# Kernel optimization log

Measured on AMD Instinct MI355X. Metric: run time of the kernel, lower is better.

## Reference

```python
import jax, jax.numpy as jnp
import numpy as np

RESO = 64            # plane_resolution
PADDING = 0.1
HID = 128            # hidden_dim
CDIM = 128           # c_dim
NBLOCKS = 5
PLANES = ((0, 2), (0, 1), (1, 2))  # xz, xy, yz column picks


def _plane_index(p, cols):
    # normalize_coordinate + coordinate2index (2d)
    xy = p[..., list(cols)] / (1.0 + PADDING + 1e-3) + 0.5
    xy = jnp.clip(xy, 0.0, 1.0 - 1e-3)
    ij = (xy * RESO).astype(jnp.int32)
    return ij[..., 0] + RESO * ij[..., 1]  # [B, T]


def _flat_idx(idx, S):
    B = idx.shape[0]
    return (idx + jnp.arange(B, dtype=idx.dtype)[:, None] * S).reshape(-1)


def _scatter_max(src, idx, S):
    # src [B,T,F], idx [B,T] -> [B,S,F]; empty bins -> 0 (torch_scatter convention)
    B, T, F = src.shape
    m = jax.ops.segment_max(src.reshape(B * T, F), _flat_idx(idx, S), num_segments=B * S)
    m = jnp.where(jnp.isfinite(m), m, jnp.zeros((), src.dtype))
    return m.reshape(B, S, F)


def _scatter_mean(src, idx, S):
    B, T, F = src.shape
    flat = _flat_idx(idx, S)
    s = jax.ops.segment_sum(src.reshape(B * T, F), flat, num_segments=B * S)
    cnt = jax.ops.segment_sum(jnp.ones((B * T,), src.dtype), flat, num_segments=B * S)
    return (s / jnp.maximum(cnt, 1.0)[:, None]).reshape(B, S, F)


def _resblock(x, w0, b0, w1, b1, ws):
    # ONet ResnetBlockFC: fc_1(relu(fc_0(relu(x)))) + shortcut(x)
    net = jax.nn.relu(x) @ w0 + b0
    dx = jax.nn.relu(net) @ w1 + b1
    return x @ ws + dx


def setup_inputs() -> dict:
    key = jax.random.key(0)
    ks = jax.random.split(key, 10)
    sc = 0.05
    return {
        "p": jax.random.normal(ks[0], (8, 20000, 3), dtype=jnp.float32),
        "fc_pos_w": jax.random.normal(ks[1], (3, 2 * HID), dtype=jnp.float32) * sc,
        "fc_pos_b": jnp.zeros((2 * HID,), jnp.float32),
        "blk0_w": jax.random.normal(ks[2], (NBLOCKS, 2 * HID, HID), dtype=jnp.float32) * sc,
        "blk0_b": jnp.zeros((NBLOCKS, HID), jnp.float32),
        "blk1_w": jax.random.normal(ks[3], (NBLOCKS, HID, HID), dtype=jnp.float32) * sc,
        "blk1_b": jnp.zeros((NBLOCKS, HID), jnp.float32),
        "blk_sc_w": jax.random.normal(ks[4], (NBLOCKS, 2 * HID, HID), dtype=jnp.float32) * sc,
        "fc_c_w": jax.random.normal(ks[5], (HID, CDIM), dtype=jnp.float32) * sc,
        "fc_c_b": jnp.zeros((CDIM,), jnp.float32),
    }


def reference(p, fc_pos_w, fc_pos_b, blk0_w, blk0_b, blk1_w, blk1_b, blk_sc_w, fc_c_w, fc_c_b):
    S = RESO * RESO
    B = p.shape[0]
    idxs = [_plane_index(p, cols) for cols in PLANES]

    net = p @ fc_pos_w + fc_pos_b                         # [B,T,2H]
    net = _resblock(net, blk0_w[0], blk0_b[0], blk1_w[0], blk1_b[0], blk_sc_w[0])
    for i in range(1, NBLOCKS):
        pooled = jnp.zeros_like(net[..., :HID])
        for idx in idxs:
            fea = _scatter_max(net, idx, S)               # [B,S,H]
            pooled = pooled + jnp.take_along_axis(fea, idx[:, :, None], axis=1)
        net = jnp.concatenate([net, pooled], axis=-1)     # [B,T,2H]
        net = _resblock(net, blk0_w[i], blk0_b[i], blk1_w[i], blk1_b[i], blk_sc_w[i])

    c = net @ fc_c_w + fc_c_b                             # [B,T,C]
    feas = []
    for idx in idxs:
        fp = _scatter_mean(c, idx, S)                     # [B,S,C]
        feas.append(fp.transpose(0, 2, 1).reshape(B, CDIM, RESO, RESO))
    return jnp.stack(feas)                                # [3,B,C,R,R] (xz, xy, yz)
```

## Files before the change

### kernel.cpp

```cpp
#include <hip/hip_runtime.h>
#include <cstdint>
#include <cstddef>

#define NP     160000
#define NB     8
#define TPB    20000
#define H      128
#define SS     4096
#define NCHUNK 625
#define NBLK   10
#define PPB    2000

typedef _Float16 half8  __attribute__((ext_vector_type(8)));
typedef _Float16 half4v __attribute__((ext_vector_type(4)));
typedef float    f32x16 __attribute__((ext_vector_type(16)));

__device__ __forceinline__ half8 reluh8(half8 x) {
  half8 z = (half8)(_Float16)0;
  return __builtin_elementwise_max(x, z);
}

__global__ __launch_bounds__(256) void k_hist(const float* __restrict__ p,
                                              int* __restrict__ idx,
                                              unsigned* __restrict__ hist) {
  __shared__ unsigned lh[SS];
  const int tid = threadIdx.x;
  const int plb = blockIdx.x % 24;
  const int blk = blockIdx.x / 24;
  const int pl = plb >> 3, b = plb & 7;
  for (int j = tid; j < SS; j += 256) lh[j] = 0;
  __syncthreads();
  const float DEN = (float)(1.0 + 0.1 + 1e-3);
  const float HI  = (float)(1.0 - 1e-3);
  const int nbase = b*TPB + blk*PPB;
  for (int j = tid; j < PPB; j += 256) {
    const int n = nbase + j;
    const float px = p[3*n], py = p[3*n+1], pz = p[3*n+2];
    float ca, cb;
    if (pl == 0)      { ca = px; cb = pz; }
    else if (pl == 1) { ca = px; cb = py; }
    else              { ca = py; cb = pz; }
    const float na = fminf(fmaxf(ca / DEN + 0.5f, 0.0f), HI);
    const float nb = fminf(fmaxf(cb / DEN + 0.5f, 0.0f), HI);
    const int bin = (int)(na * 64.0f) + 64 * (int)(nb * 64.0f);
    idx[pl*NP + n] = bin;
    atomicAdd(&lh[bin], 1u);
  }
  __syncthreads();
  unsigned* dst = hist + ((size_t)plb*NBLK + blk)*SS;
  for (int j = tid; j < SS; j += 256) dst[j] = lh[j];
}

__global__ __launch_bounds__(256) void k_scan2(unsigned* __restrict__ hist,
                                               unsigned* __restrict__ cnt,
                                               int* __restrict__ cursor) {
  __shared__ unsigned stot[SS];
  __shared__ unsigned ssum[256];
  __shared__ unsigned sbase[256];
  const int plb = blockIdx.x;
  const int tid = threadIdx.x;
  unsigned* hp = hist + (size_t)plb*NBLK*SS;
  for (int j = tid; j < SS; j += 256) {
    unsigned t = 0;
    #pragma unroll
    for (int blk = 0; blk < NBLK; ++blk) t += hp[blk*SS + j];
    stot[j] = t;
  }
  __syncthreads();
  unsigned local = 0;
  #pragma unroll
  for (int i = 0; i < 16; ++i) local += stot[tid*16 + i];
  ssum[tid] = local;
  __syncthreads();
  if (tid == 0) {
    unsigned run = 0;
    for (int i = 0; i < 256; ++i) { sbase[i] = run; run += ssum[i]; }
  }
  __syncthreads();
  unsigned run = sbase[tid];
  for (int i = 0; i < 16; ++i) {
    const int bin = tid*16 + i;
    const unsigned tot = stot[bin];
    cnt[plb*SS + bin] = tot;
    cursor[plb*SS + bin] = (int)(run + tot);
    unsigned acc = run;
    #pragma unroll
    for (int blk = 0; blk < NBLK; ++blk) {
      const unsigned c = hp[blk*SS + bin];
      hp[blk*SS + bin] = acc;
      acc += c;
    }
    run += tot;
  }
}

__global__ __launch_bounds__(256) void k_reorder2(const int* __restrict__ idx,
                                                  const unsigned* __restrict__ hist,
                                                  int* __restrict__ order) {
  __shared__ unsigned lrank[SS];
  const int tid = threadIdx.x;
  const int plb = blockIdx.x % 24;
  const int blk = blockIdx.x / 24;
  const int pl = plb >> 3, b = plb & 7;
  for (int j = tid; j < SS; j += 256) lrank[j] = 0;
  __syncthreads();
  const unsigned* bp = hist + ((size_t)plb*NBLK + blk)*SS;
  int* op = order + pl*NP + b*TPB;
  const int nbase = b*TPB + blk*PPB;
  for (int j = tid; j < PPB; j += 256) {
    const int n = nbase + j;
    const int bin = idx[pl*NP + n];
    const unsigned r = atomicAdd(&lrank[bin], 1u);
    op[bp[bin] + r] = (bin << 18) | n;
  }
}

__global__ __launch_bounds__(256) void k_wconv(const float* __restrict__ w0,
                                               const float* __restrict__ w1,
                                               const float* __restrict__ wsc,
                                               _Float16* __restrict__ wb) {
  int t = blockIdx.x*256 + threadIdx.x;
  if (t >= 51200) return;
  int L = t / 10240, r = t % 10240;
  const float* src; _Float16* dst; int q;
  if (r < 4096)      { q = r;        src = w0  + L*32768; dst = wb + L*81920;         }
  else if (r < 8192) { q = r - 4096; src = wsc + L*32768; dst = wb + L*81920 + 32768; }
  else               { q = r - 8192; src = w1  + L*16384; dst = wb + L*81920 + 65536; }
  int kt = q >> 8, nt = (q >> 6) & 3, l = q & 63;
  int k0 = kt*16 + ((l >> 5) << 3);
  int n  = nt*32 + (l & 31);
  union { _Float16 h[8]; uint4 u; } o;
  #pragma unroll
  for (int j = 0; j < 8; ++j) o.h[j] = (_Float16)src[(size_t)(k0 + j)*H + n];
  *(uint4*)(dst + (size_t)q*8) = o.u;
}

template<int OP>
__global__ __launch_bounds__(256) void k_poolA(const _Float16* __restrict__ net,
                                               const int* __restrict__ order,
                                               _Float16* __restrict__ fea,
                                               float* __restrict__ sums,
                                               float* __restrict__ pbufF,
                                               float* __restrict__ pbufL) {
  const int tid   = threadIdx.x;
  const int plb   = blockIdx.x % 24;
  const int chunk = (blockIdx.x / 24) * 8 + (tid >> 5);
  if (chunk >= NCHUNK) return;
  const int gi = tid & 31, f4 = gi << 2;
  const int pl = plb >> 3, b = plb & 7;
  const int base = pl*NP + b*TPB + chunk*32;
  const int pkv = order[base + gi];
  const int prevbin = (chunk > 0)          ? (order[base - 1] >> 18) : -1;
  const int nextbin = (chunk < NCHUNK - 1) ? (order[base + 32] >> 18) : -1;

  uint2 v[32];
  #pragma unroll
  for (int i = 0; i < 32; ++i) {
    const int pk = __shfl(pkv, i, 32);
    v[i] = *(const uint2*)&net[(size_t)(pk & 0x3FFFF)*H + f4];
  }
  __builtin_amdgcn_sched_barrier(0);

  const size_t pslot = ((size_t)plb*NCHUNK + chunk)*H + f4;
  int cur = __shfl(pkv, 0, 32) >> 18;
  int segstart = 0;
  float a0, a1, a2, a3;
  if (OP == 0) { a0 = a1 = a2 = a3 = -3.0e38f; } else { a0 = a1 = a2 = a3 = 0.f; }

  #pragma unroll
  for (int i = 0; i < 32; ++i) {
    const int bin = __shfl(pkv, i, 32) >> 18;
    if (bin != cur) {
      const bool contin = (segstart == 0) && (prevbin == cur);
      if (!contin) {
        if (OP == 0) {
          union { _Float16 h[4]; uint2 u; } o;
          o.h[0]=(_Float16)a0; o.h[1]=(_Float16)a1; o.h[2]=(_Float16)a2; o.h[3]=(_Float16)a3;
          *(uint2*)&fea[((size_t)plb*SS + cur)*H + f4] = o.u;
        } else {
          *(float4*)&sums[((size_t)plb*SS + cur)*H + f4] = make_float4(a0,a1,a2,a3);
        }
      } else {
        *(float4*)&pbufF[pslot] = make_float4(a0,a1,a2,a3);
      }
      cur = bin; segstart = i;
      if (OP == 0) { a0 = a1 = a2 = a3 = -3.0e38f; } else { a0 = a1 = a2 = a3 = 0.f; }
    }
    union { uint2 u; _Float16 h[4]; } w;
    w.u = v[i];
    if (OP == 0) {
      a0 = fmaxf(a0, (float)w.h[0]); a1 = fmaxf(a1, (float)w.h[1]);
      a2 = fmaxf(a2, (float)w.h[2]); a3 = fmaxf(a3, (float)w.h[3]);
    } else {
      a0 += (float)w.h[0]; a1 += (float)w.h[1];
      a2 += (float)w.h[2]; a3 += (float)w.h[3];
    }
  }
  const bool contin = (segstart == 0) && (prevbin == cur);
  const bool extend = (nextbin == cur);
  if (!contin && !extend) {
    if (OP == 0) {
      union { _Float16 h[4]; uint2 u; } o;
      o.h[0]=(_Float16)a0; o.h[1]=(_Float16)a1; o.h[2]=(_Float16)a2; o.h[3]=(_Float16)a3;
      *(uint2*)&fea[((size_t)plb*SS + cur)*H + f4] = o.u;
    } else {
      *(float4*)&sums[((size_t)plb*SS + cur)*H + f4] = make_float4(a0,a1,a2,a3);
    }
  } else if (contin) {
    *(float4*)&pbufF[pslot] = make_float4(a0,a1,a2,a3);
  } else {
    *(float4*)&pbufL[pslot] = make_float4(a0,a1,a2,a3);
  }
}

template<int OP>
__global__ __launch_bounds__(256) void k_poolB(const int* __restrict__ order,
                                               const int* __restrict__ cursor,
                                               _Float16* __restrict__ fea,
                                               float* __restrict__ sums,
                                               const float* __restrict__ pbufF,
                                               const float* __restrict__ pbufL) {
  const int tid = threadIdx.x;
  const int plb = blockIdx.x % 24;
  const int bnd = (blockIdx.x / 24) * 8 + (tid >> 5);
  if (bnd >= NCHUNK - 1) return;
  const int gi = tid & 31, f4 = gi << 2;
  const int pl = plb >> 3, b = plb & 7;
  const int base = pl*NP + b*TPB;
  const int pos  = (bnd + 1) * 32;
  const int binR = order[base + pos] >> 18;
  const int binL = order[base + pos - 1] >> 18;
  if (binL != binR) return;
  const int beta = binR;
  const int e = cursor[plb*SS + beta];
  const int s = (beta > 0) ? cursor[plb*SS + beta - 1] : 0;
  const int cs = s >> 5, ce = (e - 1) >> 5;
  if (cs != bnd) return;
  float4 acc = *(const float4*)&pbufL[((size_t)plb*NCHUNK + cs)*H + f4];
  #pragma unroll 4
  for (int c = cs + 1; c <= ce; ++c) {
    const float4 q = *(const float4*)&pbufF[((size_t)plb*NCHUNK + c)*H + f4];
    if (OP == 0) {
      acc.x = fmaxf(acc.x, q.x); acc.y = fmaxf(acc.y, q.y);
      acc.z = fmaxf(acc.z, q.z); acc.w = fmaxf(acc.w, q.w);
    } else {
      acc.x += q.x; acc.y += q.y; acc.z += q.z; acc.w += q.w;
    }
  }
  if (OP == 0) {
    union { _Float16 h[4]; uint2 u; } o;
    o.h[0]=(_Float16)acc.x; o.h[1]=(_Float16)acc.y;
    o.h[2]=(_Float16)acc.z; o.h[3]=(_Float16)acc.w;
    *(uint2*)&fea[((size_t)plb*SS + beta)*H + f4] = o.u;
  } else {
    *(float4*)&sums[((size_t)plb*SS + beta)*H + f4] = acc;
  }
}

template<int MODE>
__global__ __launch_bounds__(512, 6) void k_block(
    const float* __restrict__ p,
    const float* __restrict__ wpos, const float* __restrict__ bpos,
    _Float16* __restrict__ net,
    const _Float16* __restrict__ fea, const int* __restrict__ idx,
    const _Float16* __restrict__ wb,
    const float* __restrict__ b0, const float* __restrict__ b1)
{
  __shared__ char smem[49152];
  char* Xs = smem;
  char* Hs = smem + 32768;
  const int tid = threadIdx.x;
  const int n0  = blockIdx.x * 64;

  if (MODE == 0) {
    for (int j = tid; j < 64*64; j += 512) {
      int pt = j >> 6, k4 = (j & 63) << 2;
      int n = n0 + pt;
      float px = p[3*n], py = p[3*n+1], pz = p[3*n+2];
      float4 a  = *(const float4*)&bpos[k4];
      float4 wx = *(const float4*)&wpos[k4];
      float4 wy = *(const float4*)&wpos[256 + k4];
      float4 wz = *(const float4*)&wpos[512 + k4];
      a.x += px*wx.x + py*wy.x + pz*wz.x;
      a.y += px*wx.y + py*wy.y + pz*wz.y;
      a.z += px*wx.z + py*wy.z + pz*wz.z;
      a.w += px*wx.w + py*wy.w + pz*wz.w;
      union { _Float16 h[4]; uint2 u; } o;
      o.h[0] = (_Float16)a.x; o.h[1] = (_Float16)a.y;
      o.h[2] = (_Float16)a.z; o.h[3] = (_Float16)a.w;
      *(uint2*)(Xs + ((pt*512 + k4*2) ^ ((pt & 31) << 4))) = o.u;
    }
  } else {
    for (int j = tid; j < 64*32; j += 512) {
      int pt = j >> 5, k4 = (j & 31) << 2;
      int n = n0 + pt;
      int b = n / TPB;
      uint2 vleft = *(const uint2*)&net[(size_t)n*H + k4];
      union { uint2 u; half4v h; } w0g, w1g, w2g, o;
      w0g.u = *(const uint2*)&fea[(((size_t)(0*NB + b))*SS + idx[0*NP + n])*H + k4];
      w1g.u = *(const uint2*)&fea[(((size_t)(1*NB + b))*SS + idx[1*NP + n])*H + k4];
      w2g.u = *(const uint2*)&fea[(((size_t)(2*NB + b))*SS + idx[2*NP + n])*H + k4];
      o.h = (w0g.h + w1g.h) + w2g.h;
      const int sw = (pt & 31) << 4;
      *(uint2*)(Xs + ((pt*512 + k4*2) ^ sw)) = vleft;
      *(uint2*)(Xs + ((pt*512 + 256 + k4*2) ^ sw)) = o.u;
    }
  }
  __syncthreads();

  const int w  = tid >> 6;
  const int c  = w & 3;
  const int r  = w >> 2;
  const int ln = tid & 63;
  const int l5 = ln >> 5;
  const int lr = ln & 31;
  const int swx   = lr << 4;
  const int xbase = lr*512 + l5*16 + r*16384;
  const int col   = c*32 + lr;
  const _Float16* wb0 = wb;
  const _Float16* wbs = wb + 32768;
  const _Float16* wb1 = wb + 65536;

  f32x16 aR = {};
  #pragma unroll 4
  for (int kt = 0; kt < 16; ++kt) {
    half8 x  = *(const half8*)(Xs + ((xbase + kt*32) ^ swx));
    half8 rx = reluh8(x);
    half8 bw = *(const half8*)(wb0 + ((kt*4 + c)*64 + ln)*8);
    aR = __builtin_amdgcn_mfma_f32_32x32x16_f16(rx, bw, aR, 0, 0, 0);
  }
  const float bb0 = b0[col];
  #pragma unroll
  for (int reg = 0; reg < 16; ++reg) {
    const int ro  = (reg & 3) + 8*(reg >> 2) + 4*l5;
    const int row = r*32 + ro;
    const float v = fmaxf(aR[reg] + bb0, 0.f);
    *(_Float16*)(Hs + ((row*256 + col*2) ^ ((row & 15) << 4))) = (_Float16)v;
  }

  f32x16 aS = {};
  #pragma unroll 4
  for (int kt = 0; kt < 16; ++kt) {
    half8 x  = *(const half8*)(Xs + ((xbase + kt*32) ^ swx));
    half8 bs = *(const half8*)(wbs + ((kt*4 + c)*64 + ln)*8);
    aS = __builtin_amdgcn_mfma_f32_32x32x16_f16(x, bs, aS, 0, 0, 0);
  }
  __syncthreads();

  const int hbase = (r*32 + lr)*256 + l5*16;
  const int swh   = (lr & 15) << 4;
  #pragma unroll 2
  for (int kt = 0; kt < 8; ++kt) {
    half8 h  = *(const half8*)(Hs + ((hbase + kt*32) ^ swh));
    half8 bf = *(const half8*)(wb1 + ((kt*4 + c)*64 + ln)*8);
    aS = __builtin_amdgcn_mfma_f32_32x32x16_f16(h, bf, aS, 0, 0, 0);
  }

  const float bb1 = b1[col];
  #pragma unroll
  for (int reg = 0; reg < 16; ++reg) {
    const int ro = (reg & 3) + 8*(reg >> 2) + 4*l5;
    net[(size_t)(n0 + r*32 + ro)*H + col] = (_Float16)(aS[reg] + bb1);
  }
}

__global__ __launch_bounds__(256) void k_out2(const float* __restrict__ sums,
                                              const unsigned* __restrict__ cnt,
                                              const float* __restrict__ wc,
                                              const float* __restrict__ bc,
                                              float* __restrict__ out) {
  __shared__ float xa[64][132];
  const int plb = blockIdx.y;
  const int s0  = blockIdx.x << 6;
  const int tid = threadIdx.x;

  for (int j = tid; j < 64*32; j += 256) {
    int si = j >> 5, k4 = (j & 31) << 2;
    int s = s0 + si;
    float4 v = *(const float4*)&sums[((size_t)plb*SS + s)*H + k4];
    unsigned c = cnt[(size_t)plb*SS + s];
    float m = (c > 0u) ? (1.0f / (float)c) : 0.0f;
    xa[si][k4+0] = v.x*m; xa[si][k4+1] = v.y*m;
    xa[si][k4+2] = v.z*m; xa[si][k4+3] = v.w*m;
  }
  __syncthreads();

  const int fg = tid & 31;
  const int pg = tid >> 5;
  const int f4c = fg << 2;
  const int prow = pg << 3;
  float ac[8][4];
  #pragma unroll
  for (int i = 0; i < 8; ++i) { ac[i][0]=ac[i][1]=ac[i][2]=ac[i][3]=0.f; }
  #pragma unroll 4
  for (int k = 0; k < H; ++k) {
    const float4 wv = *(const float4*)&wc[(size_t)k*H + f4c];
    #pragma unroll
    for (int i = 0; i < 8; ++i) {
      const float xv = xa[prow + i][k];
      ac[i][0] += xv*wv.x; ac[i][1] += xv*wv.y; ac[i][2] += xv*wv.z; ac[i][3] += xv*wv.w;
    }
  }
  __syncthreads();
  const float4 bv = *(const float4*)&bc[f4c];
  #pragma unroll
  for (int i = 0; i < 8; ++i) {
    float4 o;
    o.x = ac[i][0] + bv.x;
    o.y = ac[i][1] + bv.y;
    o.z = ac[i][2] + bv.z;
    o.w = ac[i][3] + bv.w;
    *(float4*)&xa[prow + i][f4c] = o;
  }
  __syncthreads();

  for (int j = tid; j < H * 16; j += 256) {
    const int ch = j >> 4;
    const int s4 = (j & 15) << 2;
    float4 o;
    o.x = xa[s4 + 0][ch];
    o.y = xa[s4 + 1][ch];
    o.z = xa[s4 + 2][ch];
    o.w = xa[s4 + 3][ch];
    *(float4*)&out[((size_t)plb*H + ch)*SS + s0 + s4] = o;
  }
}

extern "C" void kernel_launch(void* const* d_in, const int* in_sizes, int n_in,
                              void* d_out, int out_size, void* d_ws, size_t ws_size,
                              hipStream_t stream) {
  (void)in_sizes; (void)n_in; (void)out_size; (void)ws_size;
  const float* p      = (const float*)d_in[0];
  const float* wpos   = (const float*)d_in[1];
  const float* bpos   = (const float*)d_in[2];
  const float* blk0w  = (const float*)d_in[3];
  const float* blk0b  = (const float*)d_in[4];
  const float* blk1w  = (const float*)d_in[5];
  const float* blk1b  = (const float*)d_in[6];
  const float* blkscw = (const float*)d_in[7];
  const float* wc     = (const float*)d_in[8];
  const float* bc     = (const float*)d_in[9];
  float* out = (float*)d_out;

  char* ws = (char*)d_ws;
  _Float16* net  = (_Float16*)ws;
  int* idx       = (int*)(ws + 40960000);
  int* order     = (int*)(ws + 42880000);
  int* cursor    = (int*)(ws + 44800000);
  unsigned* cnt  = (unsigned*)(ws + 45193216);
  _Float16* wb   = (_Float16*)(ws + 45586432);
  float* sums    = (float*)(ws + 46405632);
  float* pbufF   = (float*)(ws + 96737280);
  float* pbufL   = (float*)(ws + 104417280);
  unsigned* hist = (unsigned*)(ws + 112097280);
  _Float16* fea  = (_Float16*)d_out;

  k_hist<<<24*NBLK, 256, 0, stream>>>(p, idx, hist);
  k_scan2<<<24, 256, 0, stream>>>(hist, cnt, cursor);
  k_reorder2<<<24*NBLK, 256, 0, stream>>>(idx, hist, order);
  k_wconv<<<200, 256, 0, stream>>>(blk0w, blk1w, blkscw, wb);

  k_block<0><<<2500, 512, 0, stream>>>(p, wpos, bpos, net, nullptr, idx,
                                       wb, blk0b, blk1b);

  for (int i = 1; i < 5; ++i) {
    k_poolA<0><<<79*24, 256, 0, stream>>>(net, order, fea, nullptr, pbufF, pbufL);
    k_poolB<0><<<78*24, 256, 0, stream>>>(order, cursor, fea, nullptr, pbufF, pbufL);
    k_block<1><<<2500, 512, 0, stream>>>(nullptr, nullptr, nullptr, net, fea, idx,
                                         wb + (size_t)i*81920,
                                         blk0b + (size_t)i*H,
                                         blk1b + (size_t)i*H);
  }

  k_poolA<1><<<79*24, 256, 0, stream>>>(net, order, nullptr, sums, pbufF, pbufL);
  k_poolB<1><<<78*24, 256, 0, stream>>>(order, cursor, nullptr, sums, pbufF, pbufL);
  k_out2<<<dim3(64, 24), 256, 0, stream>>>(sums, cnt, wc, bc, out);
}
```

Measured before the change: 470.7 us.

## Make pooled resblock kernel persistent with register prefetch of next tile's gathers

The MODE 1 resblock kernel becomes a persistent kernel launched with 512 blocks that loop over the 2500 point tiles. While the MFMA work for the current tile runs, each thread loads the next tile's net rows and the three gathered plane features into registers. This is meant to hide the latency of those random gathers behind compute. Per-thread constants are hoisted out of the loop and the launch-bounds occupancy hint drops from 6 to 4, which raises register pressure and can leave tiles unevenly spread across blocks.

```diff
diff --git a/kernel.cpp b/kernel.cpp
--- a/kernel.cpp
+++ b/kernel.cpp
@@ -10,6 +10,8 @@
 #define NCHUNK 625
 #define NBLK   10
 #define PPB    2000
+#define NTILE  2500
+#define GRID1  512
 
 typedef _Float16 half8  __attribute__((ext_vector_type(8)));
 typedef _Float16 half4v __attribute__((ext_vector_type(4)));
@@ -258,7 +260,7 @@
 }
 
 template<int MODE>
-__global__ __launch_bounds__(512, 6) void k_block(
+__global__ __launch_bounds__(512, 4) void k_block(
     const float* __restrict__ p,
     const float* __restrict__ wpos, const float* __restrict__ bpos,
     _Float16* __restrict__ net,
@@ -270,9 +272,63 @@
   char* Xs = smem;
   char* Hs = smem + 32768;
   const int tid = threadIdx.x;
-  const int n0  = blockIdx.x * 64;
+
+  const int w  = tid >> 6;
+  const int c  = w & 3;
+  const int r  = w >> 2;
+  const int ln = tid & 63;
+  const int l5 = ln >> 5;
+  const int lr = ln & 31;
+  const int swx   = lr << 4;
+  const int xbase = lr*512 + l5*16 + r*16384;
+  const int col   = c*32 + lr;
+  const int hbase = (r*32 + lr)*256 + l5*16;
+  const int swh   = (lr & 15) << 4;
+  const float bb0 = b0[col];
+  const float bb1 = b1[col];
+  const _Float16* wb0 = wb;
+  const _Float16* wbs = wb + 32768;
+  const _Float16* wb1 = wb + 65536;
+
+  auto COMPUTE = [&](int n0) {
+    f32x16 aR = {};
+    #pragma unroll 4
+    for (int kt = 0; kt < 16; ++kt) {
+      half8 x  = *(const half8*)(Xs + ((xbase + kt*32) ^ swx));
+      half8 rx = reluh8(x);
+      half8 bw = *(const half8*)(wb0 + ((kt*4 + c)*64 + ln)*8);
+      aR = __builtin_amdgcn_mfma_f32_32x32x16_f16(rx, bw, aR, 0, 0, 0);
+    }
+    #pragma unroll
+    for (int reg = 0; reg < 16; ++reg) {
+      const int ro  = (reg & 3) + 8*(reg >> 2) + 4*l5;
+      const int row = r*32 + ro;
+      const float v = fmaxf(aR[reg] + bb0, 0.f);
+      *(_Float16*)(Hs + ((row*256 + col*2) ^ ((row & 15) << 4))) = (_Float16)v;
+    }
+    f32x16 aS = {};
+    #pragma unroll 4
+    for (int kt = 0; kt < 16; ++kt) {
+      half8 x  = *(const half8*)(Xs + ((xbase + kt*32) ^ swx));
+      half8 bs = *(const half8*)(wbs + ((kt*4 + c)*64 + ln)*8);
+      aS = __builtin_amdgcn_mfma_f32_32x32x16_f16(x, bs, aS, 0, 0, 0);
+    }
+    __syncthreads();
+    #pragma unroll 2
+    for (int kt = 0; kt < 8; ++kt) {
+      half8 h  = *(const half8*)(Hs + ((hbase + kt*32) ^ swh));
+      half8 bf = *(const half8*)(wb1 + ((kt*4 + c)*64 + ln)*8);
+      aS = __builtin_amdgcn_mfma_f32_32x32x16_f16(h, bf, aS, 0, 0, 0);
+    }
+    #pragma unroll
+    for (int reg = 0; reg < 16; ++reg) {
+      const int ro = (reg & 3) + 8*(reg >> 2) + 4*l5;
+      net[(size_t)(n0 + r*32 + ro)*H + col] = (_Float16)(aS[reg] + bb1);
+    }
+  };
 
   if (MODE == 0) {
+    const int n0 = blockIdx.x * 64;
     for (int j = tid; j < 64*64; j += 512) {
       int pt = j >> 6, k4 = (j & 63) << 2;
       int n = n0 + pt;
@@ -290,77 +346,45 @@
       o.h[2] = (_Float16)a.z; o.h[3] = (_Float16)a.w;
       *(uint2*)(Xs + ((pt*512 + k4*2) ^ ((pt & 31) << 4))) = o.u;
     }
-  } else {
-    for (int j = tid; j < 64*32; j += 512) {
-      int pt = j >> 5, k4 = (j & 31) << 2;
-      int n = n0 + pt;
-      int b = n / TPB;
-      uint2 vleft = *(const uint2*)&net[(size_t)n*H + k4];
-      union { uint2 u; half4v h; } w0g, w1g, w2g, o;
-      w0g.u = *(const uint2*)&fea[(((size_t)(0*NB + b))*SS + idx[0*NP + n])*H + k4];
-      w1g.u = *(const uint2*)&fea[(((size_t)(1*NB + b))*SS + idx[1*NP + n])*H + k4];
-      w2g.u = *(const uint2*)&fea[(((size_t)(2*NB + b))*SS + idx[2*NP + n])*H + k4];
-      o.h = (w0g.h + w1g.h) + w2g.h;
+    __syncthreads();
+    COMPUTE(n0);
+    return;
+  }
+
+  const int pt0 = tid >> 5;
+  const int k4  = (tid & 31) << 2;
+  uint2 pre[4][4];
+  auto LOADT = [&](int tt) {
+    #pragma unroll
+    for (int i = 0; i < 4; ++i) {
+      const int pt = pt0 + i*16;
+      const int n  = tt*64 + pt;
+      const int b  = n / TPB;
+      pre[i][0] = *(const uint2*)&net[(size_t)n*H + k4];
+      pre[i][1] = *(const uint2*)&fea[(((size_t)(0*NB + b))*SS + idx[0*NP + n])*H + k4];
+      pre[i][2] = *(const uint2*)&fea[(((size_t)(1*NB + b))*SS + idx[1*NP + n])*H + k4];
+      pre[i][3] = *(const uint2*)&fea[(((size_t)(2*NB + b))*SS + idx[2*NP + n])*H + k4];
+    }
+  };
+
+  int t = blockIdx.x;
+  LOADT(t);
+  while (t < NTILE) {
+    #pragma unroll
+    for (int i = 0; i < 4; ++i) {
+      const int pt = pt0 + i*16;
+      union { uint2 u; half4v h; } g0, g1, g2, o;
+      g0.u = pre[i][1]; g1.u = pre[i][2]; g2.u = pre[i][3];
+      o.h = (g0.h + g1.h) + g2.h;
       const int sw = (pt & 31) << 4;
-      *(uint2*)(Xs + ((pt*512 + k4*2) ^ sw)) = vleft;
+      *(uint2*)(Xs + ((pt*512 + k4*2) ^ sw)) = pre[i][0];
       *(uint2*)(Xs + ((pt*512 + 256 + k4*2) ^ sw)) = o.u;
     }
-  }
-  __syncthreads();
-
-  const int w  = tid >> 6;
-  const int c  = w & 3;
-  const int r  = w >> 2;
-  const int ln = tid & 63;
-  const int l5 = ln >> 5;
-  const int lr = ln & 31;
-  const int swx   = lr << 4;
-  const int xbase = lr*512 + l5*16 + r*16384;
-  const int col   = c*32 + lr;
-  const _Float16* wb0 = wb;
-  const _Float16* wbs = wb + 32768;
-  const _Float16* wb1 = wb + 65536;
-
-  f32x16 aR = {};
-  #pragma unroll 4
-  for (int kt = 0; kt < 16; ++kt) {
-    half8 x  = *(const half8*)(Xs + ((xbase + kt*32) ^ swx));
-    half8 rx = reluh8(x);
-    half8 bw = *(const half8*)(wb0 + ((kt*4 + c)*64 + ln)*8);
-    aR = __builtin_amdgcn_mfma_f32_32x32x16_f16(rx, bw, aR, 0, 0, 0);
-  }
-  const float bb0 = b0[col];
-  #pragma unroll
-  for (int reg = 0; reg < 16; ++reg) {
-    const int ro  = (reg & 3) + 8*(reg >> 2) + 4*l5;
-    const int row = r*32 + ro;
-    const float v = fmaxf(aR[reg] + bb0, 0.f);
-    *(_Float16*)(Hs + ((row*256 + col*2) ^ ((row & 15) << 4))) = (_Float16)v;
-  }
-
-  f32x16 aS = {};
-  #pragma unroll 4
-  for (int kt = 0; kt < 16; ++kt) {
-    half8 x  = *(const half8*)(Xs + ((xbase + kt*32) ^ swx));
-    half8 bs = *(const half8*)(wbs + ((kt*4 + c)*64 + ln)*8);
-    aS = __builtin_amdgcn_mfma_f32_32x32x16_f16(x, bs, aS, 0, 0, 0);
-  }
-  __syncthreads();
-
-  const int hbase = (r*32 + lr)*256 + l5*16;
-  const int swh   = (lr & 15) << 4;
-  #pragma unroll 2
-  for (int kt = 0; kt < 8; ++kt) {
-    half8 h  = *(const half8*)(Hs + ((hbase + kt*32) ^ swh));
-    half8 bf = *(const half8*)(wb1 + ((kt*4 + c)*64 + ln)*8);
-    aS = __builtin_amdgcn_mfma_f32_32x32x16_f16(h, bf, aS, 0, 0, 0);
-  }
-
-  const float bb1 = b1[col];
-  #pragma unroll
-  for (int reg = 0; reg < 16; ++reg) {
-    const int ro = (reg & 3) + 8*(reg >> 2) + 4*l5;
-    net[(size_t)(n0 + r*32 + ro)*H + col] = (_Float16)(aS[reg] + bb1);
+    const int tn = t + (int)gridDim.x;
+    if (tn < NTILE) LOADT(tn);
+    __syncthreads();
+    COMPUTE(t * 64);
+    t = tn;
   }
 }
 
@@ -466,10 +490,10 @@
   for (int i = 1; i < 5; ++i) {
     k_poolA<0><<<79*24, 256, 0, stream>>>(net, order, fea, nullptr, pbufF, pbufL);
     k_poolB<0><<<78*24, 256, 0, stream>>>(order, cursor, fea, nullptr, pbufF, pbufL);
-    k_block<1><<<2500, 512, 0, stream>>>(nullptr, nullptr, nullptr, net, fea, idx,
-                                         wb + (size_t)i*81920,
-                                         blk0b + (size_t)i*H,
-                                         blk1b + (size_t)i*H);
+    k_block<1><<<GRID1, 512, 0, stream>>>(nullptr, nullptr, nullptr, net, fea, idx,
+                                          wb + (size_t)i*81920,
+                                          blk0b + (size_t)i*H,
+                                          blk1b + (size_t)i*H);
   }
 
   k_poolA<1><<<79*24, 256, 0, stream>>>(net, order, nullptr, sums, pbufF, pbufL);
```

Result: slower. 486.5 us (+3.4%).
